# Optimization experiments

Measured on AMD Instinct MI355X. Metric: run time of the kernel, lower is better.

## Reference

```python
import jax, jax.numpy as jnp
import numpy as np

N = 100_000      # nodes
E = 1_200_000    # edges per graph (avg degree 12)
D = 64           # args.hidden
PROP_STEP = 8
LAM = 1.0
ALP = 1.0 / (LAM + 1.0)   # args.alp <= 0 -> 1/(lam+1)
LAM0 = 1.0
K = 4
LAM_K = 0.5


def setup_inputs() -> dict:
    key = jax.random.key(0)
    k0, k1, k2, k3, k4 = jax.random.split(key, 5)
    x = jax.random.normal(k0, (N, D), dtype=jnp.float32)
    src0 = jax.random.randint(k1, (E,), 0, N, dtype=jnp.int32)
    # ensure every node has in-degree >= 1 (no isolated dst nodes)
    dst0 = jnp.concatenate([jnp.arange(N, dtype=jnp.int32),
                            jax.random.randint(k2, (E - N,), 0, N, dtype=jnp.int32)])
    src1 = jax.random.randint(k3, (E,), 0, N, dtype=jnp.int32)
    dst1 = jnp.concatenate([jnp.arange(N, dtype=jnp.int32),
                            jax.random.randint(k4, (E - N,), 0, N, dtype=jnp.int32)])
    return {"x": x, "src0": src0, "dst0": dst0, "src1": src1, "dst1": dst1}


def _in_degrees(dst):
    # DGL in_degrees(): count of incoming edges per node
    return jax.ops.segment_sum(jnp.ones(dst.shape, jnp.float32), dst, num_segments=N)


def _normalized_AX(src, dst, inv_sqrt_deg, Y):
    # Y <- D^{-1/2} A D^{-1/2} Y  (edge weight w = 1)
    Yn = Y * inv_sqrt_deg                                    # [N, D]
    agg = jax.ops.segment_sum(Yn[src], dst, num_segments=N)  # gather/scatter SpMM
    return agg * inv_sqrt_deg


def reference(x, src0, dst0, src1, dst1):
    deg0 = _in_degrees(dst0)
    deg1 = _in_degrees(dst1)
    # D^{-1/2} with inf -> 0 (as in D_power_X)
    inv0 = jnp.where(deg0 > 0, deg0 ** -0.5, 0.0)[:, None]
    inv1 = jnp.where(deg1 > 0, deg1 ** -0.5, 0.0)[:, None]
    D0 = deg0[:, None]
    D1 = deg1[:, None]
    Y = x
    for _ in range(PROP_STEP):
        nAX0 = _normalized_AX(src0, dst0, inv0, Y)
        nAX1 = _normalized_AX(src1, dst1, inv1, Y)
        Y = Y - ALP * (LAM0 * (Y - x) / (D0 + D1)
                       + LAM * (Y - nAX0)
                       - (LAM_K / K) * (Y - nAX1))
    return Y
```

## Files before the change

### kernel.cpp

```cpp
#include <hip/hip_runtime.h>
#include <hip/hip_fp16.h>

#define NN 100000
#define NE 1200000
#define DIM 64
#define NBINS 391
#define NBE 128
#define CHUNK (NE / NBE)
#define NBLK ((NN + 255) / 256)
#define NPH 7


__global__ void __launch_bounds__(256) bin_count(const int* __restrict__ dst0,
                                                 const int* __restrict__ dst1,
                                                 int* __restrict__ blk_cnt) {
    __shared__ int c[NBINS];
    int t = threadIdx.x;
    for (int i = t; i < NBINS; i += 256) c[i] = 0;
    __syncthreads();
    int lo = blockIdx.x * CHUNK, hi = lo + CHUNK;
    for (int e = lo + t; e < hi; e += 256) {
        atomicAdd(&c[dst0[e] >> 8], 1);
        atomicAdd(&c[dst1[e] >> 8], 1);
    }
    __syncthreads();
    for (int i = t; i < NBINS; i += 256) blk_cnt[blockIdx.x * NBINS + i] = c[i];
}

__global__ void __launch_bounds__(512) bin_scan(const int* __restrict__ blk_cnt,
                                                int* __restrict__ bin_start) {
    __shared__ int tot[512];
    int t = threadIdx.x;
    int s = 0;
    if (t < NBINS)
        for (int b = 0; b < NBE; ++b) s += blk_cnt[b * NBINS + t];
    tot[t] = s;
    __syncthreads();
    for (int off = 1; off < 512; off <<= 1) {
        int v = (t >= off) ? tot[t - off] : 0;
        __syncthreads();
        tot[t] += v;
        __syncthreads();
    }
    if (t <= NBINS) bin_start[t] = tot[t] - s;
}

__global__ void __launch_bounds__(NBE) blk_base_k(const int* __restrict__ blk_cnt,
                                                  const int* __restrict__ bin_start,
                                                  int* __restrict__ blk_base) {
    __shared__ int s[NBE];
    int b = blockIdx.x, t = threadIdx.x;
    int v = blk_cnt[t * NBINS + b];
    s[t] = v;
    __syncthreads();
    for (int off = 1; off < NBE; off <<= 1) {
        int x = (t >= off) ? s[t - off] : 0;
        __syncthreads();
        s[t] += x;
        __syncthreads();
    }
    blk_base[t * NBINS + b] = bin_start[b] + s[t] - v;
}

__global__ void __launch_bounds__(256) bin_permute(const int* __restrict__ src0,
                                                   const int* __restrict__ dst0,
                                                   const int* __restrict__ src1,
                                                   const int* __restrict__ dst1,
                                                   const int* __restrict__ blk_base,
                                                   unsigned int* __restrict__ binned) {
    __shared__ int off[NBINS];
    int t = threadIdx.x;
    for (int i = t; i < NBINS; i += 256) off[i] = blk_base[blockIdx.x * NBINS + i];
    __syncthreads();
    int lo = blockIdx.x * CHUNK, hi = lo + CHUNK;
    for (int e = lo + t; e < hi; e += 256) {
        int s = src0[e], d = dst0[e];
        int p = atomicAdd(&off[d >> 8], 1);
        binned[p] = (unsigned)s | ((unsigned)(d & 255) << 18);
        s = src1[e]; d = dst1[e];
        p = atomicAdd(&off[d >> 8], 1);
        binned[p] = (unsigned)s | (1u << 17) | ((unsigned)(d & 255) << 18);
    }
}

__global__ void __launch_bounds__(256) deg_count(const unsigned int* __restrict__ binned,
                                                 const int* __restrict__ bin_start,
                                                 int* __restrict__ deg0,
                                                 int* __restrict__ deg1) {
    __shared__ int dg[512];
    int b = blockIdx.x, t = threadIdx.x;
    dg[t] = 0; dg[t + 256] = 0;
    __syncthreads();
    int lo = bin_start[b], hi = bin_start[b + 1];
    for (int i = lo + t; i < hi; i += 256) {
        unsigned r = binned[i];
        int dlow = (r >> 18) & 255, g = (r >> 17) & 1;
        atomicAdd(&dg[(dlow << 1) | g], 1);
    }
    __syncthreads();
    int n = b * 256 + t;
    if (n < NN) { deg0[n] = dg[t << 1]; deg1[n] = dg[(t << 1) | 1]; }
}

__global__ void __launch_bounds__(256) scan_l1(const int* __restrict__ deg0,
                                               const int* __restrict__ deg1,
                                               int* __restrict__ rs, int* __restrict__ dp,
                                               int* __restrict__ bs) {
    __shared__ int s0[256];
    int t = threadIdx.x;
    int n = blockIdx.x * 256 + t;
    int a = 0;
    if (n < NN) a = (deg0[n] + deg1[n] + 7) & ~7;
    s0[t] = a;
    __syncthreads();
    for (int off = 1; off < 256; off <<= 1) {
        int x0 = (t >= off) ? s0[t - off] : 0;
        __syncthreads();
        s0[t] += x0;
        __syncthreads();
    }
    if (n < NN) { rs[n] = s0[t] - a; dp[n] = a; }
    if (t == 255) bs[blockIdx.x] = s0[255];
}

__global__ void __launch_bounds__(512) scan_l2(int* __restrict__ bs) {
    __shared__ int s0[512];
    int t = threadIdx.x;
    int a = (t < NBLK) ? bs[t] : 0;
    s0[t] = a;
    __syncthreads();
    for (int off = 1; off < 512; off <<= 1) {
        int x0 = (t >= off) ? s0[t - off] : 0;
        __syncthreads();
        s0[t] += x0;
        __syncthreads();
    }
    if (t < NBLK) bs[t] = s0[t] - a;
}

__global__ void __launch_bounds__(256) scan_l3(int* __restrict__ rs, const int* __restrict__ bs) {
    int n = blockIdx.x * 256 + threadIdx.x;
    if (n < NN) rs[n] += bs[blockIdx.x];
}

__global__ void node_params(const int* __restrict__ deg0, const int* __restrict__ deg1,
                            float2* __restrict__ nsc, float* __restrict__ sc,
                            float* __restrict__ cy) {
    int n = blockIdx.x * blockDim.x + threadIdx.x;
    if (n < NN) {
        int a = deg0[n], b = deg1[n];
        nsc[n] = make_float2((a > 0) ? 0.5f * rsqrtf((float)a) : 0.0f,
                             (b > 0) ? -0.0625f * rsqrtf((float)b) : 0.0f);
        int s = a + b;
        float rD = (s > 0) ? 1.0f / (float)s : 0.0f;
        sc[n] = 0.5625f - 0.5f * rD;
        cy[n] = 0.5f * rD;
    }
}

__global__ void __launch_bounds__(256) csr_scatter(const unsigned int* __restrict__ binned,
                                                   const int* __restrict__ bin_start,
                                                   const int* __restrict__ rs,
                                                   const int* __restrict__ deg0,
                                                   const int* __restrict__ deg1,
                                                   const float2* __restrict__ nsc,
                                                   int* __restrict__ es) {
    __shared__ int hist[8 * 256];
    __shared__ int rsl[256];
    __shared__ int degsum[256];
    __shared__ float2 nscl[256];
    __shared__ float lutw[128];
    int b = blockIdx.x, t = threadIdx.x;
    int n = b * 256 + t;
    rsl[t]  = (n < NN) ? rs[n] : 0;
    nscl[t] = (n < NN) ? nsc[n] : make_float2(0.0f, 0.0f);
    if (t < 128) lutw[t] = (t == 0) ? 0.0f : rsqrtf((float)t);
    for (int i = t; i < 8 * 256; i += 256) hist[i] = 0;
    __syncthreads();
    int lo = bin_start[b], hi = bin_start[b + 1];
    for (int i = lo + t; i < hi; i += 256) {
        unsigned r = binned[i];
        int ph = (r & 0x1FFFF) >> 14;
        atomicAdd(&hist[ph * 256 + ((r >> 18) & 255)], 1);
    }
    __syncthreads();
    {
        int acc = 0;
        for (int ph = 0; ph < NPH; ++ph) {
            int v = hist[ph * 256 + t];
            hist[ph * 256 + t] = acc;
            acc += v;
        }
        degsum[t] = acc;
    }
    __syncthreads();
    for (int i = lo + t; i < hi; i += 256) {
        unsigned r = binned[i];
        int sN = r & 0x1FFFF, g = (r >> 17) & 1, dlow = (r >> 18) & 255;
        int ph = sN >> 14;
        int p = atomicAdd(&hist[ph * 256 + dlow], 1);
        int dgv = g ? deg1[sN] : deg0[sN];
        float2 nn = nscl[dlow];
        float wf = (g ? nn.y : nn.x) * lutw[dgv & 127];
        unsigned u = (unsigned)__half_as_ushort(__float2half(wf));
        es[rsl[dlow] + p] = (int)((((u + 1u) >> 1) << 17) | (unsigned)sN);
    }
    __syncthreads();
    if (n < NN) {
        int base = rsl[t], ds = degsum[t], dpv = (ds + 7) & ~7;
        for (int i = base + ds; i < base + dpv; ++i) es[i] = 0;
    }
}

__global__ void convert_x(const float* __restrict__ X, const float* __restrict__ cy,
                          __half* __restrict__ HA, __half* __restrict__ BX) {
    int i = blockIdx.x * blockDim.x + threadIdx.x;
    if (i < NN * DIM / 4) {
        float4 v = ((const float4*)X)[i];
        float c = cy[i >> 4];
        ushort4 a, b;
        a.x = __half_as_ushort(__float2half(v.x));
        a.y = __half_as_ushort(__float2half(v.y));
        a.z = __half_as_ushort(__float2half(v.z));
        a.w = __half_as_ushort(__float2half(v.w));
        b.x = __half_as_ushort(__float2half(v.x * c));
        b.y = __half_as_ushort(__float2half(v.y * c));
        b.z = __half_as_ushort(__float2half(v.z * c));
        b.w = __half_as_ushort(__float2half(v.w * c));
        ((ushort4*)HA)[i] = a;
        ((ushort4*)BX)[i] = b;
    }
}

__device__ __forceinline__ float4 h4f(ushort4 v) {
    return make_float4(__half2float(__ushort_as_half(v.x)),
                       __half2float(__ushort_as_half(v.y)),
                       __half2float(__ushort_as_half(v.z)),
                       __half2float(__ushort_as_half(v.w)));
}

__device__ __forceinline__ float wdec(int r) {
    return __half2float(__ushort_as_half((unsigned short)(((unsigned)r >> 16) & 0xFFFEu)));
}

__global__ void __launch_bounds__(256) step_kernel(
    const __half* __restrict__ Yh, const __half* __restrict__ BX,
    const int* __restrict__ rs, const int* __restrict__ dp,
    const int* __restrict__ es, const float* __restrict__ sc,
    __half* __restrict__ Yho, float* __restrict__ Ffo)
{
    int node = blockIdx.x * 4 + (threadIdx.x >> 6);
    int lane = threadIdx.x & 63;
    int sub  = lane >> 4;
    int fl   = lane & 15;
    int un = __builtin_amdgcn_readfirstlane(node);
    int s  = __builtin_amdgcn_readfirstlane(rs[un]);
    int c  = __builtin_amdgcn_readfirstlane(dp[un]);

    const int2* ep = (const int2*)(es + s) + sub;

    float4 acc = make_float4(0.0f, 0.0f, 0.0f, 0.0f);
    int2 rA = ep[0];
    int2 rB = ep[4];
    ushort4 gA0 = *(const ushort4*)(Yh + (size_t)(rA.x & 0x1FFFF) * DIM + 4 * fl);
    ushort4 gA1 = *(const ushort4*)(Yh + (size_t)(rA.y & 0x1FFFF) * DIM + 4 * fl);
    for (int i = 0; i < c; i += 8) {
        int2 rC = ep[(i >> 1) + 8];
        ushort4 gB0 = *(const ushort4*)(Yh + (size_t)(rB.x & 0x1FFFF) * DIM + 4 * fl);
        ushort4 gB1 = *(const ushort4*)(Yh + (size_t)(rB.y & 0x1FFFF) * DIM + 4 * fl);
        float w0 = wdec(rA.x);
        float w1 = wdec(rA.y);
        float4 f0 = h4f(gA0), f1 = h4f(gA1);
        acc.x = fmaf(f0.x, w0, acc.x);
        acc.y = fmaf(f0.y, w0, acc.y);
        acc.z = fmaf(f0.z, w0, acc.z);
        acc.w = fmaf(f0.w, w0, acc.w);
        acc.x = fmaf(f1.x, w1, acc.x);
        acc.y = fmaf(f1.y, w1, acc.y);
        acc.z = fmaf(f1.z, w1, acc.z);
        acc.w = fmaf(f1.w, w1, acc.w);
        rA = rB; rB = rC; gA0 = gB0; gA1 = gB1;
    }
    acc.x += __shfl_xor(acc.x, 16); acc.x += __shfl_xor(acc.x, 32);
    acc.y += __shfl_xor(acc.y, 16); acc.y += __shfl_xor(acc.y, 32);
    acc.z += __shfl_xor(acc.z, 16); acc.z += __shfl_xor(acc.z, 32);
    acc.w += __shfl_xor(acc.w, 16); acc.w += __shfl_xor(acc.w, 32);

    if (sub == 0) {
        float4 y  = h4f(*(const ushort4*)(Yh + (size_t)un * DIM + 4 * fl));
        float4 bx = h4f(*(const ushort4*)(BX + (size_t)un * DIM + 4 * fl));
        float scl = sc[un];
        float o0 = fmaf(scl, y.x, bx.x) + acc.x;
        float o1 = fmaf(scl, y.y, bx.y) + acc.y;
        float o2 = fmaf(scl, y.z, bx.z) + acc.z;
        float o3 = fmaf(scl, y.w, bx.w) + acc.w;
        if (Ffo) {
            *(float4*)(Ffo + (size_t)un * DIM + 4 * fl) = make_float4(o0, o1, o2, o3);
        } else {
            ushort4 ov;
            ov.x = __half_as_ushort(__float2half(o0));
            ov.y = __half_as_ushort(__float2half(o1));
            ov.z = __half_as_ushort(__float2half(o2));
            ov.w = __half_as_ushort(__float2half(o3));
            *(ushort4*)(Yho + (size_t)un * DIM + 4 * fl) = ov;
        }
    }
}

extern "C" void kernel_launch(void* const* d_in, const int* in_sizes, int n_in,
                              void* d_out, int out_size, void* d_ws, size_t ws_size,
                              hipStream_t stream) {
    const float* x   = (const float*)d_in[0];
    const int* src0  = (const int*)d_in[1];
    const int* dst0  = (const int*)d_in[2];
    const int* src1  = (const int*)d_in[3];
    const int* dst1  = (const int*)d_in[4];
    float* out = (float*)d_out;

    char* ws = (char*)d_ws;
    size_t off = 0;
    auto alloc = [&](size_t bytes) -> void* {
        void* p = ws + off;
        off += (bytes + 255) & ~(size_t)255;
        return p;
    };

    const size_t ES_CAP = (size_t)2 * NE + 8 * NN + 256;

    __half* HA   = (__half*)alloc((size_t)NN * DIM * 2);
    __half* HB   = (__half*)alloc((size_t)NN * DIM * 2);
    __half* BX   = (__half*)alloc((size_t)NN * DIM * 2);
    unsigned int* binned = (unsigned int*)alloc((size_t)2 * NE * 4);
    int*    es   = (int*)alloc(ES_CAP * 4);
    int*    blk_cnt  = (int*)alloc((size_t)NBE * NBINS * 4);
    int*    blk_base = (int*)alloc((size_t)NBE * NBINS * 4);
    int*    bin_st   = (int*)alloc((size_t)(NBINS + 1) * 4);
    int*    deg0 = (int*)alloc((size_t)NN * 4);
    int*    deg1 = (int*)alloc((size_t)NN * 4);
    int*    rs   = (int*)alloc((size_t)NN * 4);
    int*    dp   = (int*)alloc((size_t)NN * 4);
    float2* nsc  = (float2*)alloc((size_t)NN * 8);
    float*  sc   = (float*)alloc((size_t)NN * 4);
    float*  cy   = (float*)alloc((size_t)NN * 4);
    int*    bs   = (int*)alloc((size_t)NBLK * 4);

    const int TB = 256;
    bin_count<<<NBE, 256, 0, stream>>>(dst0, dst1, blk_cnt);
    bin_scan<<<1, 512, 0, stream>>>(blk_cnt, bin_st);
    blk_base_k<<<NBINS, NBE, 0, stream>>>(blk_cnt, bin_st, blk_base);
    bin_permute<<<NBE, 256, 0, stream>>>(src0, dst0, src1, dst1, blk_base, binned);
    deg_count<<<NBINS, 256, 0, stream>>>(binned, bin_st, deg0, deg1);
    scan_l1<<<NBLK, 256, 0, stream>>>(deg0, deg1, rs, dp, bs);
    scan_l2<<<1, 512, 0, stream>>>(bs);
    scan_l3<<<NBLK, 256, 0, stream>>>(rs, bs);
    node_params<<<(NN + TB - 1) / TB, TB, 0, stream>>>(deg0, deg1, nsc, sc, cy);
    csr_scatter<<<NBINS, 256, 0, stream>>>(binned, bin_st, rs, deg0, deg1, nsc, es);
    convert_x<<<(NN * DIM / 4 + TB - 1) / TB, TB, 0, stream>>>(x, cy, HA, BX);

    int grid = NN / 4;
    for (int i = 0; i < 8; ++i) {
        const __half* hin = (i & 1) ? HB : HA;
        __half* hout = (i & 1) ? HA : HB;
        float* fout = (i == 7) ? out : nullptr;
        step_kernel<<<grid, TB, 0, stream>>>(hin, BX, rs, dp, es, sc, hout, fout);
    }
}
```

Before: 490.9 us.

## Split feature dimension into four quarter-planes for cache-local gathers

Stores Y and BX as four planes of 16 half-precision features per node and launches four times as many step blocks, each covering one quarter of the features. Each gather now fetches 32 bytes from a 3.2 MB plane instead of 128 bytes from the full array, so the gathered data can stay in L2 or the MALL. Edge lists are padded to 16 so each lane group handles one edge per iteration. In exchange, every edge index is read four times, there are more shuffle reductions, and the extra padding adds work.

New measurement: 1.133 ms. 131% more time.

```diff
diff --git a/kernel.cpp b/kernel.cpp
--- a/kernel.cpp
+++ b/kernel.cpp
@@ -4,6 +4,8 @@
 #define NN 100000
 #define NE 1200000
 #define DIM 64
+#define QF 16
+#define NQ 4
 #define NBINS 391
 #define NBE 128
 #define CHUNK (NE / NBE)
@@ -110,7 +112,7 @@
     int t = threadIdx.x;
     int n = blockIdx.x * 256 + t;
     int a = 0;
-    if (n < NN) a = (deg0[n] + deg1[n] + 7) & ~7;
+    if (n < NN) a = (deg0[n] + deg1[n] + 15) & ~15;
     s0[t] = a;
     __syncthreads();
     for (int off = 1; off < 256; off <<= 1) {
@@ -207,7 +209,7 @@
     }
     __syncthreads();
     if (n < NN) {
-        int base = rsl[t], ds = degsum[t], dpv = (ds + 7) & ~7;
+        int base = rsl[t], ds = degsum[t], dpv = (ds + 15) & ~15;
         for (int i = base + ds; i < base + dpv; ++i) es[i] = 0;
     }
 }
@@ -215,9 +217,11 @@
 __global__ void convert_x(const float* __restrict__ X, const float* __restrict__ cy,
                           __half* __restrict__ HA, __half* __restrict__ BX) {
     int i = blockIdx.x * blockDim.x + threadIdx.x;
-    if (i < NN * DIM / 4) {
+    if (i < NN * 16) {
+        int n = i >> 4, j = i & 15;
         float4 v = ((const float4*)X)[i];
-        float c = cy[i >> 4];
+        float c = cy[n];
+        size_t dsti = (size_t)(j >> 2) * NN * QF + (size_t)n * QF + (j & 3) * 4;
         ushort4 a, b;
         a.x = __half_as_ushort(__float2half(v.x));
         a.y = __half_as_ushort(__float2half(v.y));
@@ -227,8 +231,8 @@
         b.y = __half_as_ushort(__float2half(v.y * c));
         b.z = __half_as_ushort(__float2half(v.z * c));
         b.w = __half_as_ushort(__float2half(v.w * c));
-        ((ushort4*)HA)[i] = a;
-        ((ushort4*)BX)[i] = b;
+        *(ushort4*)(HA + dsti) = a;
+        *(ushort4*)(BX + dsti) = b;
     }
 }
 
@@ -244,65 +248,68 @@
 }
 
 __global__ void __launch_bounds__(256) step_kernel(
-    const __half* __restrict__ Yh, const __half* __restrict__ BX,
+    const __half* __restrict__ Yh, const __half* __restrict__ BXq,
     const int* __restrict__ rs, const int* __restrict__ dp,
     const int* __restrict__ es, const float* __restrict__ sc,
     __half* __restrict__ Yho, float* __restrict__ Ffo)
 {
-    int node = blockIdx.x * 4 + (threadIdx.x >> 6);
+    const int bpq = NN / 4;
+    int q  = blockIdx.x / bpq;
+    int nb = blockIdx.x - q * bpq;
+    int node = nb * 4 + (threadIdx.x >> 6);
     int lane = threadIdx.x & 63;
-    int sub  = lane >> 4;
-    int fl   = lane & 15;
+    int sub  = lane >> 2;
+    int fl   = lane & 3;
     int un = __builtin_amdgcn_readfirstlane(node);
     int s  = __builtin_amdgcn_readfirstlane(rs[un]);
     int c  = __builtin_amdgcn_readfirstlane(dp[un]);
 
-    const int2* ep = (const int2*)(es + s) + sub;
+    const __half* Yq = Yh + (size_t)q * NN * QF;
+    const int* ep = es + s + sub;
 
     float4 acc = make_float4(0.0f, 0.0f, 0.0f, 0.0f);
-    int2 rA = ep[0];
-    int2 rB = ep[4];
-    ushort4 gA0 = *(const ushort4*)(Yh + (size_t)(rA.x & 0x1FFFF) * DIM + 4 * fl);
-    ushort4 gA1 = *(const ushort4*)(Yh + (size_t)(rA.y & 0x1FFFF) * DIM + 4 * fl);
-    for (int i = 0; i < c; i += 8) {
-        int2 rC = ep[(i >> 1) + 8];
-        ushort4 gB0 = *(const ushort4*)(Yh + (size_t)(rB.x & 0x1FFFF) * DIM + 4 * fl);
-        ushort4 gB1 = *(const ushort4*)(Yh + (size_t)(rB.y & 0x1FFFF) * DIM + 4 * fl);
-        float w0 = wdec(rA.x);
-        float w1 = wdec(rA.y);
-        float4 f0 = h4f(gA0), f1 = h4f(gA1);
-        acc.x = fmaf(f0.x, w0, acc.x);
-        acc.y = fmaf(f0.y, w0, acc.y);
-        acc.z = fmaf(f0.z, w0, acc.z);
-        acc.w = fmaf(f0.w, w0, acc.w);
-        acc.x = fmaf(f1.x, w1, acc.x);
-        acc.y = fmaf(f1.y, w1, acc.y);
-        acc.z = fmaf(f1.z, w1, acc.z);
-        acc.w = fmaf(f1.w, w1, acc.w);
-        rA = rB; rB = rC; gA0 = gB0; gA1 = gB1;
-    }
+    int rA = ep[0];
+    int rB = ep[16];
+    ushort4 gA = *(const ushort4*)(Yq + (size_t)(rA & 0x1FFFF) * QF + 4 * fl);
+    for (int i = 0; i < c; i += 16) {
+        int rC = ep[i + 32];
+        ushort4 gB = *(const ushort4*)(Yq + (size_t)(rB & 0x1FFFF) * QF + 4 * fl);
+        float w = wdec(rA);
+        float4 f = h4f(gA);
+        acc.x = fmaf(f.x, w, acc.x);
+        acc.y = fmaf(f.y, w, acc.y);
+        acc.z = fmaf(f.z, w, acc.z);
+        acc.w = fmaf(f.w, w, acc.w);
+        rA = rB; rB = rC; gA = gB;
+    }
+    acc.x += __shfl_xor(acc.x, 4);  acc.x += __shfl_xor(acc.x, 8);
     acc.x += __shfl_xor(acc.x, 16); acc.x += __shfl_xor(acc.x, 32);
+    acc.y += __shfl_xor(acc.y, 4);  acc.y += __shfl_xor(acc.y, 8);
     acc.y += __shfl_xor(acc.y, 16); acc.y += __shfl_xor(acc.y, 32);
+    acc.z += __shfl_xor(acc.z, 4);  acc.z += __shfl_xor(acc.z, 8);
     acc.z += __shfl_xor(acc.z, 16); acc.z += __shfl_xor(acc.z, 32);
+    acc.w += __shfl_xor(acc.w, 4);  acc.w += __shfl_xor(acc.w, 8);
     acc.w += __shfl_xor(acc.w, 16); acc.w += __shfl_xor(acc.w, 32);
 
     if (sub == 0) {
-        float4 y  = h4f(*(const ushort4*)(Yh + (size_t)un * DIM + 4 * fl));
-        float4 bx = h4f(*(const ushort4*)(BX + (size_t)un * DIM + 4 * fl));
+        size_t qi = (size_t)q * NN * QF + (size_t)un * QF + 4 * fl;
+        float4 y  = h4f(*(const ushort4*)(Yh + qi));
+        float4 bx = h4f(*(const ushort4*)(BXq + qi));
         float scl = sc[un];
         float o0 = fmaf(scl, y.x, bx.x) + acc.x;
         float o1 = fmaf(scl, y.y, bx.y) + acc.y;
         float o2 = fmaf(scl, y.z, bx.z) + acc.z;
         float o3 = fmaf(scl, y.w, bx.w) + acc.w;
         if (Ffo) {
-            *(float4*)(Ffo + (size_t)un * DIM + 4 * fl) = make_float4(o0, o1, o2, o3);
+            *(float4*)(Ffo + (size_t)un * DIM + q * QF + 4 * fl) =
+                make_float4(o0, o1, o2, o3);
         } else {
             ushort4 ov;
             ov.x = __half_as_ushort(__float2half(o0));
             ov.y = __half_as_ushort(__float2half(o1));
             ov.z = __half_as_ushort(__float2half(o2));
             ov.w = __half_as_ushort(__float2half(o3));
-            *(ushort4*)(Yho + (size_t)un * DIM + 4 * fl) = ov;
+            *(ushort4*)(Yho + qi) = ov;
         }
     }
 }
@@ -325,7 +332,7 @@
         return p;
     };
 
-    const size_t ES_CAP = (size_t)2 * NE + 8 * NN + 256;
+    const size_t ES_CAP = (size_t)2 * NE + 16 * NN + 256;
 
     __half* HA   = (__half*)alloc((size_t)NN * DIM * 2);
     __half* HB   = (__half*)alloc((size_t)NN * DIM * 2);
@@ -355,9 +362,9 @@
     scan_l3<<<NBLK, 256, 0, stream>>>(rs, bs);
     node_params<<<(NN + TB - 1) / TB, TB, 0, stream>>>(deg0, deg1, nsc, sc, cy);
     csr_scatter<<<NBINS, 256, 0, stream>>>(binned, bin_st, rs, deg0, deg1, nsc, es);
-    convert_x<<<(NN * DIM / 4 + TB - 1) / TB, TB, 0, stream>>>(x, cy, HA, BX);
-
-    int grid = NN / 4;
+    convert_x<<<(NN * 16 + TB - 1) / TB, TB, 0, stream>>>(x, cy, HA, BX);
+
+    int grid = (NN / 4) * NQ;
     for (int i = 0; i < 8; ++i) {
         const __half* hin = (i & 1) ? HB : HA;
         __half* hout = (i & 1) ? HA : HB;
```
